# Kernel tuning notes

Hardware: AMD Instinct MI355X
Metric: run time of the kernel (lower is better)

## Reference

```python
import jax, jax.numpy as jnp
import numpy as np

C_IN = 256
K = 4
C_QK = C_IN // K  # 64


def setup_inputs() -> dict:
    key = jax.random.key(0)
    ks = jax.random.split(key, 9)
    B, C, H, W = 4, C_IN, 64, 64
    s = 0.02
    return {
        "x": jax.random.normal(ks[0], (B, C, H, W), dtype=jnp.float32),
        # 1x1 convs stored as dense [out, in] matrices (kernel_size=1)
        "wq": jax.random.normal(ks[1], (C_QK, C), dtype=jnp.float32) * s,
        "bq": jax.random.normal(ks[2], (C_QK,), dtype=jnp.float32) * s,
        "wk": jax.random.normal(ks[3], (C_QK, C), dtype=jnp.float32) * s,
        "bk": jax.random.normal(ks[4], (C_QK,), dtype=jnp.float32) * s,
        "wv": jax.random.normal(ks[5], (C, C), dtype=jnp.float32) * s,
        "bv": jax.random.normal(ks[6], (C,), dtype=jnp.float32) * s,
        "wg": jax.random.normal(ks[7], (C, C), dtype=jnp.float32) * s,
        "bg": jax.random.normal(ks[8], (C,), dtype=jnp.float32) * s,
    }


def reference(x, wq, bq, wk, bk, wv, bv, wg, bg):
    B, C, H, W = x.shape
    N = H * W
    xf = x.reshape(B, C, N)  # [B, C, N]
    # 1x1 conv == per-pixel linear over channels
    q = jnp.einsum("oc,bcn->bon", wq, xf) + bq[None, :, None]  # [B, Cqk, N]
    k = jnp.einsum("oc,bcn->bon", wk, xf) + bk[None, :, None]  # [B, Cqk, N]
    v = jnp.einsum("oc,bcn->bon", wv, xf) + bv[None, :, None]  # [B, C, N]
    # energy[b, n, m] = <q[:, n], k[:, m]>  (n = query pos, m = key pos)
    energy = jnp.einsum("bon,bom->bnm", q, k)  # [B, N, N]
    energy = jax.nn.elu(energy) / N
    # out[b, c, m] = sum_n v[b, c, n] * energy[b, n, m]
    out = jnp.einsum("bcn,bnm->bcm", v, energy).reshape(B, C, H, W)
    out = jnp.einsum("oc,bchw->bohw", wg, out) + bg[None, :, None, None]
    return out
```

## Files before the change

### kernel.cpp

```cpp
#include <hip/hip_runtime.h>

#define B_ 4
#define C_ 256
#define CQK 64
#define N_ 4096
#define SEG 2
#define SEGN (N_ / SEG)
#define NB 128
#define ITERS (SEGN / NB)
#define TS 512

typedef _Float16 f16;
typedef __attribute__((ext_vector_type(8))) _Float16 f16x8;
typedef __attribute__((ext_vector_type(4))) _Float16 f16x4;
typedef __attribute__((ext_vector_type(4))) float f32x4;
typedef __attribute__((ext_vector_type(4))) float float4v;

#define TILE_OFF(l15, quad) ((l15) * 32 + (quad) * 8)

__global__ __launch_bounds__(256) void prep_w(
    const float* __restrict__ wq, const float* __restrict__ wk,
    const float* __restrict__ wv, const float* __restrict__ wg,
    f16* __restrict__ WQt, f16* __restrict__ WKt, f16* __restrict__ WVt,
    f16* __restrict__ WGt) {
  int chunk = blockIdx.x * 256 + threadIdx.x;
  if (chunk >= 20480) return;
  const float* src;
  f16* dst;
  int lo;
  if (chunk < 2048) { src = wq; dst = WQt; lo = chunk * 8; }
  else if (chunk < 4096) { src = wk; dst = WKt; lo = (chunk - 2048) * 8; }
  else if (chunk < 12288) { src = wv; dst = WVt; lo = (chunk - 4096) * 8; }
  else { src = wg; dst = WGt; lo = (chunk - 12288) * 8; }
  int o = lo >> 8, k = lo & 255;
  f16x8 v;
#pragma unroll
  for (int j = 0; j < 8; j++) v[j] = (f16)src[lo + j];
  *(f16x8*)(dst + ((size_t)(o >> 4) * 8 + (k >> 5)) * TS + (o & 15) * 32 + (k & 31)) = v;
}

__global__ __launch_bounds__(256) void proj(
    const float* __restrict__ x, const f16* __restrict__ WQt,
    const f16* __restrict__ WKt, const f16* __restrict__ WVt,
    const float* __restrict__ bq, const float* __restrict__ bk,
    const float* __restrict__ bv, f16* __restrict__ QTt, f16* __restrict__ KTt,
    f16* __restrict__ Vt) {
  __shared__ float xs[32][257];
  __shared__ f16 xt[2][8][16 * 36];
  int nx = blockIdx.x;
  int n0 = nx * 32;
  int b = blockIdx.y;
  int tid = threadIdx.x, lane = tid & 63, w = tid >> 6;
  int l15 = lane & 15, quad = lane >> 4;
  const float* xb = x + (size_t)b * C_ * N_;

  {
    int a = tid & 7;
    int crow = tid >> 3;
#pragma unroll
    for (int p = 0; p < 8; p++) {
      int c = p * 32 + crow;
      float4v vv = *(const float4v*)(xb + (size_t)c * N_ + n0 + a * 4);
      int nn = a * 4;
      xs[nn][c] = vv[0];
      xs[nn + 1][c] = vv[1];
      xs[nn + 2][c] = vv[2];
      xs[nn + 3][c] = vv[3];
    }
  }
  __syncthreads();
#pragma unroll
  for (int nt = 0; nt < 2; nt++) {
#pragma unroll
    for (int kk = 0; kk < 2; kk++) {
      int kt = 2 * w + kk;
      f16x8 v;
#pragma unroll
      for (int j = 0; j < 8; j++)
        v[j] = (f16)xs[16 * nt + l15][kt * 32 + quad * 8 + j];
      *(f16x8*)(&xt[nt][kt][l15 * 36 + quad * 8]) = v;
    }
  }
  __syncthreads();

  f32x4 acc[6][2];
#pragma unroll
  for (int j = 0; j < 6; j++)
#pragma unroll
    for (int nt = 0; nt < 2; nt++) acc[j][nt] = (f32x4){0.f, 0.f, 0.f, 0.f};

#pragma unroll
  for (int kt = 0; kt < 8; kt++) {
    f16x8 xf[2];
#pragma unroll
    for (int nt = 0; nt < 2; nt++)
      xf[nt] = *(const f16x8*)(&xt[nt][kt][l15 * 36 + quad * 8]);
#pragma unroll
    for (int j = 0; j < 6; j++) {
      int g = w * 6 + j;
      const f16* Wt;
      int ot;
      bool isV = g < 16;
      if (isV) { Wt = WVt; ot = g; }
      else if (g < 20) { Wt = WQt; ot = g - 16; }
      else { Wt = WKt; ot = g - 20; }
      f16x8 wf = *(const f16x8*)(Wt + ((size_t)ot * 8 + kt) * TS + TILE_OFF(l15, quad));
#pragma unroll
      for (int nt = 0; nt < 2; nt++)
        acc[j][nt] = isV
            ? __builtin_amdgcn_mfma_f32_16x16x32_f16(xf[nt], wf, acc[j][nt], 0, 0, 0)
            : __builtin_amdgcn_mfma_f32_16x16x32_f16(wf, xf[nt], acc[j][nt], 0, 0, 0);
    }
  }

  f16* vbout = Vt + (size_t)b * C_ * N_;
#pragma unroll
  for (int j = 0; j < 6; j++) {
    int g = w * 6 + j;
    if (g < 16) {
      float bvv = bv[16 * g + l15];
#pragma unroll
      for (int nt = 0; nt < 2; nt++) {
        f16x4 vals;
#pragma unroll
        for (int r = 0; r < 4; r++) vals[r] = (f16)(acc[j][nt][r] + bvv);
        *(f16x4*)(vbout + ((size_t)g * 128 + nx) * TS + l15 * 32 + 16 * nt +
                  4 * quad) = vals;
      }
    } else {
      int oq = (g < 20) ? (g - 16) : (g - 20);
      const float* bias = (g < 20) ? bq : bk;
      f16* ob = ((g < 20) ? QTt : KTt) + (size_t)b * N_ * CQK;
#pragma unroll
      for (int nt = 0; nt < 2; nt++) {
        f16x4 vals;
#pragma unroll
        for (int r = 0; r < 4; r++)
          vals[r] = (f16)(acc[j][nt][r] + bias[16 * oq + 4 * quad + r]);
        *(f16x4*)(ob + ((size_t)(2 * nx + nt) * 2 + (oq >> 1)) * TS + l15 * 32 +
                  16 * (oq & 1) + 4 * quad) = vals;
      }
    }
  }
}

__global__ __launch_bounds__(256, 2) void attn(const f16* __restrict__ qt,
                                               const f16* __restrict__ kt,
                                               const f16* __restrict__ v,
                                               const f16* __restrict__ WGt,
                                               f16* __restrict__ part) {
  __shared__ __align__(16) f16 sPt[2][64][128];
  int m0 = blockIdx.x * 64;
  int seg = blockIdx.y;
  int b = blockIdx.z;
  int tid = threadIdx.x, lane = tid & 63, w = tid >> 6;
  int l15 = lane & 15, quad = lane >> 4;
  const f16* qtb = qt + (size_t)b * N_ * CQK;
  const f16* ktb = kt + (size_t)b * N_ * CQK;
  const f16* vb = v + (size_t)b * C_ * N_;

  f32x4 oacc[4][4];
#pragma unroll
  for (int ct = 0; ct < 4; ct++)
#pragma unroll
    for (int mt = 0; mt < 4; mt++) oacc[ct][mt] = (f32x4){0.f, 0.f, 0.f, 0.f};

  f16x8 kf[4][2];
#pragma unroll
  for (int mt = 0; mt < 4; mt++)
#pragma unroll
    for (int ks = 0; ks < 2; ks++)
      kf[mt][ks] = *(const f16x8*)(ktb + ((size_t)((m0 >> 4) + mt) * 2 + ks) * TS +
                                   TILE_OFF(l15, quad));

  f16x8 qf[2][2];
  {
    int nq = seg * SEGN;
#pragma unroll
    for (int nt = 0; nt < 2; nt++)
#pragma unroll
      for (int ks = 0; ks < 2; ks++)
        qf[nt][ks] = *(const f16x8*)(qtb +
                                     ((size_t)((nq >> 4) + 2 * w + nt) * 2 + ks) * TS +
                                     TILE_OFF(l15, quad));
  }

  for (int it = 0; it < ITERS; it++) {
    int n0 = seg * SEGN + it * NB;
    f16x8 vfA[2][4];
#pragma unroll
    for (int ks = 0; ks < 2; ks++)
#pragma unroll
      for (int ct = 0; ct < 4; ct++)
        vfA[ks][ct] = *(const f16x8*)(vb +
                                      ((size_t)(4 * w + ct) * 128 + (n0 >> 5) + ks) * TS +
                                      TILE_OFF(l15, quad));

    char* buf = (char*)sPt[it & 1];
#pragma unroll
    for (int nt = 0; nt < 2; nt++) {
      f32x4 sacc[4];
#pragma unroll
      for (int mt = 0; mt < 4; mt++) sacc[mt] = (f32x4){0.f, 0.f, 0.f, 0.f};
#pragma unroll
      for (int ks = 0; ks < 2; ks++)
#pragma unroll
        for (int mt = 0; mt < 4; mt++)
          sacc[mt] = __builtin_amdgcn_mfma_f32_16x16x32_f16(qf[nt][ks], kf[mt][ks],
                                                            sacc[mt], 0, 0, 0);
#pragma unroll
      for (int mt = 0; mt < 4; mt++) {
        f16x4 p;
#pragma unroll
        for (int r = 0; r < 4; r++) {
          float s = sacc[mt][r];
          p[r] = (f16)(s > 0.0f ? s : (__expf(s) - 1.0f));
        }
        int row = 16 * mt + l15;
        int colb = (64 * w + 32 * nt + 8 * quad) ^ ((row & 7) << 4);
        *(f16x4*)(buf + row * 256 + colb) = p;
      }
    }
    __syncthreads();

    f16x8 vfB[2][4];
    f16x8 pa[4];
#pragma unroll
    for (int mt = 0; mt < 4; mt++) {
      int row = 16 * mt + l15;
      pa[mt] = *(const f16x8*)(buf + row * 256 + ((quad * 16) ^ ((row & 7) << 4)));
    }
#pragma unroll
    for (int ks = 0; ks < 2; ks++)
#pragma unroll
      for (int ct = 0; ct < 4; ct++)
        vfB[ks][ct] = *(const f16x8*)(vb + ((size_t)(4 * w + ct) * 128 + (n0 >> 5) +
                                            2 + ks) * TS +
                                      TILE_OFF(l15, quad));
#pragma unroll
    for (int ct = 0; ct < 4; ct++)
#pragma unroll
      for (int mt = 0; mt < 4; mt++)
        oacc[ct][mt] = __builtin_amdgcn_mfma_f32_16x16x32_f16(vfA[0][ct], pa[mt],
                                                              oacc[ct][mt], 0, 0, 0);
    if (it + 1 < ITERS) {
      int nq = n0 + NB;
#pragma unroll
      for (int nt = 0; nt < 2; nt++)
#pragma unroll
        for (int ks = 0; ks < 2; ks++)
          qf[nt][ks] = *(const f16x8*)(qtb +
                                       ((size_t)((nq >> 4) + 2 * w + nt) * 2 + ks) * TS +
                                       TILE_OFF(l15, quad));
    }
#pragma unroll
    for (int mt = 0; mt < 4; mt++) {
      int row = 16 * mt + l15;
      pa[mt] = *(const f16x8*)(buf + row * 256 + ((64 + quad * 16) ^ ((row & 7) << 4)));
    }
#pragma unroll
    for (int ct = 0; ct < 4; ct++)
#pragma unroll
      for (int mt = 0; mt < 4; mt++)
        oacc[ct][mt] = __builtin_amdgcn_mfma_f32_16x16x32_f16(vfA[1][ct], pa[mt],
                                                              oacc[ct][mt], 0, 0, 0);
#pragma unroll
    for (int mt = 0; mt < 4; mt++) {
      int row = 16 * mt + l15;
      pa[mt] = *(const f16x8*)(buf + row * 256 + ((128 + quad * 16) ^ ((row & 7) << 4)));
    }
#pragma unroll
    for (int ct = 0; ct < 4; ct++)
#pragma unroll
      for (int mt = 0; mt < 4; mt++)
        oacc[ct][mt] = __builtin_amdgcn_mfma_f32_16x16x32_f16(vfB[0][ct], pa[mt],
                                                              oacc[ct][mt], 0, 0, 0);
#pragma unroll
    for (int mt = 0; mt < 4; mt++) {
      int row = 16 * mt + l15;
      pa[mt] = *(const f16x8*)(buf + row * 256 + ((192 + quad * 16) ^ ((row & 7) << 4)));
    }
#pragma unroll
    for (int ct = 0; ct < 4; ct++)
#pragma unroll
      for (int mt = 0; mt < 4; mt++)
        oacc[ct][mt] = __builtin_amdgcn_mfma_f32_16x16x32_f16(vfB[1][ct], pa[mt],
                                                              oacc[ct][mt], 0, 0, 0);
  }

  __syncthreads();
  f16* obuf = (f16*)sPt;
#pragma unroll
  for (int ct = 0; ct < 4; ct++) {
#pragma unroll
    for (int mt = 0; mt < 4; mt++) {
      f16x4 vals;
#pragma unroll
      for (int r = 0; r < 4; r++)
        vals[r] = (f16)(oacc[ct][mt][r] * (1.0f / (float)N_));
      *(f16x4*)(obuf + (mt * 8 + 2 * w + (ct >> 1)) * TS + l15 * 32 +
                16 * (ct & 1) + 4 * quad) = vals;
    }
  }
  __syncthreads();
  f32x4 accO[4][4];
#pragma unroll
  for (int ot = 0; ot < 4; ot++)
#pragma unroll
    for (int mt = 0; mt < 4; mt++) accO[ot][mt] = (f32x4){0.f, 0.f, 0.f, 0.f};
#pragma unroll
  for (int kt = 0; kt < 8; kt++) {
    f16x8 bO[4];
#pragma unroll
    for (int mt = 0; mt < 4; mt++)
      bO[mt] = *(const f16x8*)(obuf + (mt * 8 + kt) * TS + TILE_OFF(l15, quad));
#pragma unroll
    for (int ot = 0; ot < 4; ot++) {
      f16x8 af = *(const f16x8*)(WGt + ((size_t)(4 * w + ot) * 8 + kt) * TS +
                                 TILE_OFF(l15, quad));
#pragma unroll
      for (int mt = 0; mt < 4; mt++)
        accO[ot][mt] = __builtin_amdgcn_mfma_f32_16x16x32_f16(af, bO[mt], accO[ot][mt], 0, 0, 0);
    }
  }
  f16* pb = part + ((size_t)(seg * B_ + b) * C_) * N_;
#pragma unroll
  for (int ot = 0; ot < 4; ot++) {
#pragma unroll
    for (int mt = 0; mt < 4; mt++) {
      int m = m0 + 16 * mt + l15;
#pragma unroll
      for (int r = 0; r < 4; r++) {
        int o = 64 * w + 16 * ot + 4 * quad + r;
        pb[(size_t)o * N_ + m] = (f16)accO[ot][mt][r];
      }
    }
  }
}

__global__ __launch_bounds__(256) void combine(const f16* __restrict__ part,
                                               const float* __restrict__ bg,
                                               float* __restrict__ out) {
  size_t i = ((size_t)blockIdx.x * 256 + threadIdx.x) * 8;
  f16x8 p0 = *(const f16x8*)(part + i);
  f16x8 p1 = *(const f16x8*)(part + (size_t)B_ * C_ * N_ + i);
  float bgo = bg[(i >> 12) & 255];
  float4v r0, r1;
#pragma unroll
  for (int j = 0; j < 4; j++) r0[j] = (float)p0[j] + (float)p1[j] + bgo;
#pragma unroll
  for (int j = 0; j < 4; j++) r1[j] = (float)p0[4 + j] + (float)p1[4 + j] + bgo;
  *(float4v*)(out + i) = r0;
  *(float4v*)(out + i + 4) = r1;
}

extern "C" void kernel_launch(void* const* d_in, const int* in_sizes, int n_in,
                              void* d_out, int out_size, void* d_ws, size_t ws_size,
                              hipStream_t stream) {
  const float* x = (const float*)d_in[0];
  const float* wq = (const float*)d_in[1];
  const float* bq = (const float*)d_in[2];
  const float* wk = (const float*)d_in[3];
  const float* bk = (const float*)d_in[4];
  const float* wv = (const float*)d_in[5];
  const float* bv = (const float*)d_in[6];
  const float* wg = (const float*)d_in[7];
  const float* bg = (const float*)d_in[8];
  float* out = (float*)d_out;

  char* ws = (char*)d_ws;
  f16* QTt = (f16*)ws; ws += (size_t)B_ * N_ * CQK * sizeof(f16);
  f16* KTt = (f16*)ws; ws += (size_t)B_ * N_ * CQK * sizeof(f16);
  f16* Vt  = (f16*)ws; ws += (size_t)B_ * C_ * N_ * sizeof(f16);
  f16* WQt = (f16*)ws; ws += (size_t)CQK * C_ * sizeof(f16);
  f16* WKt = (f16*)ws; ws += (size_t)CQK * C_ * sizeof(f16);
  f16* WVt = (f16*)ws; ws += (size_t)C_ * C_ * sizeof(f16);
  f16* WGt = (f16*)ws; ws += (size_t)C_ * C_ * sizeof(f16);
  f16* PART = (f16*)ws; ws += (size_t)SEG * B_ * C_ * N_ * sizeof(f16);

  prep_w<<<dim3(80), 256, 0, stream>>>(wq, wk, wv, wg, WQt, WKt, WVt, WGt);
  proj<<<dim3(N_ / 32, B_), 256, 0, stream>>>(x, WQt, WKt, WVt, bq, bk, bv,
                                              QTt, KTt, Vt);
  attn<<<dim3(N_ / 64, SEG, B_), 256, 0, stream>>>(QTt, KTt, Vt, WGt, PART);
  combine<<<dim3(2048), 256, 0, stream>>>(PART, bg, out);
}
```

Measured before the change: 164.5 us.

## Drop weight prep kernel and process two key chunks per barrier in attention

Removes the separate prep_w launch. proj and attn now read the fp32 weights directly and convert them to f16 fragments inline. The attention main loop is unrolled by two: scores for two 128-wide n-chunks are computed into a 4-deep shared buffer before a single __syncthreads, which halves barrier count and gives more room to overlap V loads with MFMA work. In exchange it raises register pressure from the extra Q and V fragments, doubles LDS use, and adds redundant fp32 weight loads and conversions in every block.

```diff
diff --git a/kernel.cpp b/kernel.cpp
--- a/kernel.cpp
+++ b/kernel.cpp
@@ -18,30 +18,18 @@
 
 #define TILE_OFF(l15, quad) ((l15) * 32 + (quad) * 8)
 
-__global__ __launch_bounds__(256) void prep_w(
-    const float* __restrict__ wq, const float* __restrict__ wk,
-    const float* __restrict__ wv, const float* __restrict__ wg,
-    f16* __restrict__ WQt, f16* __restrict__ WKt, f16* __restrict__ WVt,
-    f16* __restrict__ WGt) {
-  int chunk = blockIdx.x * 256 + threadIdx.x;
-  if (chunk >= 20480) return;
-  const float* src;
-  f16* dst;
-  int lo;
-  if (chunk < 2048) { src = wq; dst = WQt; lo = chunk * 8; }
-  else if (chunk < 4096) { src = wk; dst = WKt; lo = (chunk - 2048) * 8; }
-  else if (chunk < 12288) { src = wv; dst = WVt; lo = (chunk - 4096) * 8; }
-  else { src = wg; dst = WGt; lo = (chunk - 12288) * 8; }
-  int o = lo >> 8, k = lo & 255;
-  f16x8 v;
-#pragma unroll
-  for (int j = 0; j < 8; j++) v[j] = (f16)src[lo + j];
-  *(f16x8*)(dst + ((size_t)(o >> 4) * 8 + (k >> 5)) * TS + (o & 15) * 32 + (k & 31)) = v;
+__device__ __forceinline__ f16x8 ldw_f32(const float* __restrict__ Wp) {
+  float4v a0 = *(const float4v*)Wp;
+  float4v a1 = *(const float4v*)(Wp + 4);
+  f16x8 r;
+#pragma unroll
+  for (int j = 0; j < 4; j++) { r[j] = (f16)a0[j]; r[4 + j] = (f16)a1[j]; }
+  return r;
 }
 
 __global__ __launch_bounds__(256) void proj(
-    const float* __restrict__ x, const f16* __restrict__ WQt,
-    const f16* __restrict__ WKt, const f16* __restrict__ WVt,
+    const float* __restrict__ x, const float* __restrict__ wq,
+    const float* __restrict__ wk, const float* __restrict__ wv,
     const float* __restrict__ bq, const float* __restrict__ bk,
     const float* __restrict__ bv, f16* __restrict__ QTt, f16* __restrict__ KTt,
     f16* __restrict__ Vt) {
@@ -98,13 +86,13 @@
 #pragma unroll
     for (int j = 0; j < 6; j++) {
       int g = w * 6 + j;
-      const f16* Wt;
-      int ot;
+      const float* Wsrc;
+      int orow;
       bool isV = g < 16;
-      if (isV) { Wt = WVt; ot = g; }
-      else if (g < 20) { Wt = WQt; ot = g - 16; }
-      else { Wt = WKt; ot = g - 20; }
-      f16x8 wf = *(const f16x8*)(Wt + ((size_t)ot * 8 + kt) * TS + TILE_OFF(l15, quad));
+      if (isV) { Wsrc = wv; orow = 16 * g + l15; }
+      else if (g < 20) { Wsrc = wq; orow = 16 * (g - 16) + l15; }
+      else { Wsrc = wk; orow = 16 * (g - 20) + l15; }
+      f16x8 wf = ldw_f32(Wsrc + (size_t)orow * C_ + kt * 32 + quad * 8);
 #pragma unroll
       for (int nt = 0; nt < 2; nt++)
         acc[j][nt] = isV
@@ -147,9 +135,9 @@
 __global__ __launch_bounds__(256, 2) void attn(const f16* __restrict__ qt,
                                                const f16* __restrict__ kt,
                                                const f16* __restrict__ v,
-                                               const f16* __restrict__ WGt,
+                                               const float* __restrict__ wg,
                                                f16* __restrict__ part) {
-  __shared__ __align__(16) f16 sPt[2][64][128];
+  __shared__ __align__(16) f16 sPt[4][64][128];
   int m0 = blockIdx.x * 64;
   int seg = blockIdx.y;
   int b = blockIdx.z;
@@ -173,30 +161,35 @@
       kf[mt][ks] = *(const f16x8*)(ktb + ((size_t)((m0 >> 4) + mt) * 2 + ks) * TS +
                                    TILE_OFF(l15, quad));
 
-  f16x8 qf[2][2];
+  f16x8 qf[2][2][2];
   {
-    int nq = seg * SEGN;
-#pragma unroll
-    for (int nt = 0; nt < 2; nt++)
-#pragma unroll
-      for (int ks = 0; ks < 2; ks++)
-        qf[nt][ks] = *(const f16x8*)(qtb +
-                                     ((size_t)((nq >> 4) + 2 * w + nt) * 2 + ks) * TS +
-                                     TILE_OFF(l15, quad));
-  }
-
-  for (int it = 0; it < ITERS; it++) {
+    int base = (seg * SEGN) >> 4;
+#pragma unroll
+    for (int cc = 0; cc < 2; cc++)
+#pragma unroll
+      for (int nt = 0; nt < 2; nt++)
+#pragma unroll
+        for (int ks = 0; ks < 2; ks++)
+          qf[cc][nt][ks] =
+              *(const f16x8*)(qtb + ((size_t)(base + cc * 8 + 2 * w + nt) * 2 + ks) * TS +
+                              TILE_OFF(l15, quad));
+  }
+
+  for (int it2 = 0; it2 < ITERS / 2; it2++) {
+    int it = 2 * it2;
     int n0 = seg * SEGN + it * NB;
-    f16x8 vfA[2][4];
+    int nc = n0 >> 5;
+    char* buf0 = (char*)sPt[it & 3];
+    char* buf1 = (char*)sPt[(it + 1) & 3];
+
+    f16x8 vA0[2][4];
 #pragma unroll
     for (int ks = 0; ks < 2; ks++)
 #pragma unroll
       for (int ct = 0; ct < 4; ct++)
-        vfA[ks][ct] = *(const f16x8*)(vb +
-                                      ((size_t)(4 * w + ct) * 128 + (n0 >> 5) + ks) * TS +
+        vA0[ks][ct] = *(const f16x8*)(vb + ((size_t)(4 * w + ct) * 128 + nc + ks) * TS +
                                       TILE_OFF(l15, quad));
 
-    char* buf = (char*)sPt[it & 1];
 #pragma unroll
     for (int nt = 0; nt < 2; nt++) {
       f32x4 sacc[4];
@@ -206,7 +199,7 @@
       for (int ks = 0; ks < 2; ks++)
 #pragma unroll
         for (int mt = 0; mt < 4; mt++)
-          sacc[mt] = __builtin_amdgcn_mfma_f32_16x16x32_f16(qf[nt][ks], kf[mt][ks],
+          sacc[mt] = __builtin_amdgcn_mfma_f32_16x16x32_f16(qf[0][nt][ks], kf[mt][ks],
                                                             sacc[mt], 0, 0, 0);
 #pragma unroll
       for (int mt = 0; mt < 4; mt++) {
@@ -218,73 +211,159 @@
         }
         int row = 16 * mt + l15;
         int colb = (64 * w + 32 * nt + 8 * quad) ^ ((row & 7) << 4);
-        *(f16x4*)(buf + row * 256 + colb) = p;
+        *(f16x4*)(buf0 + row * 256 + colb) = p;
       }
     }
+
+    f16x8 vB0[2][4];
+#pragma unroll
+    for (int ks = 0; ks < 2; ks++)
+#pragma unroll
+      for (int ct = 0; ct < 4; ct++)
+        vB0[ks][ct] = *(const f16x8*)(vb + ((size_t)(4 * w + ct) * 128 + nc + 2 + ks) * TS +
+                                      TILE_OFF(l15, quad));
+
+#pragma unroll
+    for (int nt = 0; nt < 2; nt++) {
+      f32x4 sacc[4];
+#pragma unroll
+      for (int mt = 0; mt < 4; mt++) sacc[mt] = (f32x4){0.f, 0.f, 0.f, 0.f};
+#pragma unroll
+      for (int ks = 0; ks < 2; ks++)
+#pragma unroll
+        for (int mt = 0; mt < 4; mt++)
+          sacc[mt] = __builtin_amdgcn_mfma_f32_16x16x32_f16(qf[1][nt][ks], kf[mt][ks],
+                                                            sacc[mt], 0, 0, 0);
+#pragma unroll
+      for (int mt = 0; mt < 4; mt++) {
+        f16x4 p;
+#pragma unroll
+        for (int r = 0; r < 4; r++) {
+          float s = sacc[mt][r];
+          p[r] = (f16)(s > 0.0f ? s : (__expf(s) - 1.0f));
+        }
+        int row = 16 * mt + l15;
+        int colb = (64 * w + 32 * nt + 8 * quad) ^ ((row & 7) << 4);
+        *(f16x4*)(buf1 + row * 256 + colb) = p;
+      }
+    }
     __syncthreads();
 
-    f16x8 vfB[2][4];
     f16x8 pa[4];
-#pragma unroll
-    for (int mt = 0; mt < 4; mt++) {
-      int row = 16 * mt + l15;
-      pa[mt] = *(const f16x8*)(buf + row * 256 + ((quad * 16) ^ ((row & 7) << 4)));
+    f16x8 vA1[2][4];
+#pragma unroll
+    for (int mt = 0; mt < 4; mt++) {
+      int row = 16 * mt + l15;
+      pa[mt] = *(const f16x8*)(buf0 + row * 256 + ((quad * 16) ^ ((row & 7) << 4)));
     }
 #pragma unroll
     for (int ks = 0; ks < 2; ks++)
 #pragma unroll
       for (int ct = 0; ct < 4; ct++)
-        vfB[ks][ct] = *(const f16x8*)(vb + ((size_t)(4 * w + ct) * 128 + (n0 >> 5) +
-                                            2 + ks) * TS +
+        vA1[ks][ct] = *(const f16x8*)(vb + ((size_t)(4 * w + ct) * 128 + nc + 4 + ks) * TS +
                                       TILE_OFF(l15, quad));
 #pragma unroll
     for (int ct = 0; ct < 4; ct++)
 #pragma unroll
       for (int mt = 0; mt < 4; mt++)
-        oacc[ct][mt] = __builtin_amdgcn_mfma_f32_16x16x32_f16(vfA[0][ct], pa[mt],
-                                                              oacc[ct][mt], 0, 0, 0);
-    if (it + 1 < ITERS) {
-      int nq = n0 + NB;
-#pragma unroll
-      for (int nt = 0; nt < 2; nt++)
-#pragma unroll
-        for (int ks = 0; ks < 2; ks++)
-          qf[nt][ks] = *(const f16x8*)(qtb +
-                                       ((size_t)((nq >> 4) + 2 * w + nt) * 2 + ks) * TS +
-                                       TILE_OFF(l15, quad));
-    }
-#pragma unroll
-    for (int mt = 0; mt < 4; mt++) {
-      int row = 16 * mt + l15;
-      pa[mt] = *(const f16x8*)(buf + row * 256 + ((64 + quad * 16) ^ ((row & 7) << 4)));
-    }
-#pragma unroll
-    for (int ct = 0; ct < 4; ct++)
-#pragma unroll
-      for (int mt = 0; mt < 4; mt++)
-        oacc[ct][mt] = __builtin_amdgcn_mfma_f32_16x16x32_f16(vfA[1][ct], pa[mt],
-                                                              oacc[ct][mt], 0, 0, 0);
-#pragma unroll
-    for (int mt = 0; mt < 4; mt++) {
-      int row = 16 * mt + l15;
-      pa[mt] = *(const f16x8*)(buf + row * 256 + ((128 + quad * 16) ^ ((row & 7) << 4)));
-    }
-#pragma unroll
-    for (int ct = 0; ct < 4; ct++)
-#pragma unroll
-      for (int mt = 0; mt < 4; mt++)
-        oacc[ct][mt] = __builtin_amdgcn_mfma_f32_16x16x32_f16(vfB[0][ct], pa[mt],
-                                                              oacc[ct][mt], 0, 0, 0);
-#pragma unroll
-    for (int mt = 0; mt < 4; mt++) {
-      int row = 16 * mt + l15;
-      pa[mt] = *(const f16x8*)(buf + row * 256 + ((192 + quad * 16) ^ ((row & 7) << 4)));
-    }
-#pragma unroll
-    for (int ct = 0; ct < 4; ct++)
-#pragma unroll
-      for (int mt = 0; mt < 4; mt++)
-        oacc[ct][mt] = __builtin_amdgcn_mfma_f32_16x16x32_f16(vfB[1][ct], pa[mt],
+        oacc[ct][mt] = __builtin_amdgcn_mfma_f32_16x16x32_f16(vA0[0][ct], pa[mt],
+                                                              oacc[ct][mt], 0, 0, 0);
+    if (it2 + 1 < ITERS / 2) {
+      int base = ((seg * SEGN) >> 4) + (it + 2) * 8;
+#pragma unroll
+      for (int cc = 0; cc < 2; cc++)
+#pragma unroll
+        for (int nt = 0; nt < 2; nt++)
+#pragma unroll
+          for (int ks = 0; ks < 2; ks++)
+            qf[cc][nt][ks] =
+                *(const f16x8*)(qtb + ((size_t)(base + cc * 8 + 2 * w + nt) * 2 + ks) * TS +
+                                TILE_OFF(l15, quad));
+    }
+#pragma unroll
+    for (int mt = 0; mt < 4; mt++) {
+      int row = 16 * mt + l15;
+      pa[mt] = *(const f16x8*)(buf0 + row * 256 + ((64 + quad * 16) ^ ((row & 7) << 4)));
+    }
+#pragma unroll
+    for (int ct = 0; ct < 4; ct++)
+#pragma unroll
+      for (int mt = 0; mt < 4; mt++)
+        oacc[ct][mt] = __builtin_amdgcn_mfma_f32_16x16x32_f16(vA0[1][ct], pa[mt],
+                                                              oacc[ct][mt], 0, 0, 0);
+#pragma unroll
+    for (int mt = 0; mt < 4; mt++) {
+      int row = 16 * mt + l15;
+      pa[mt] = *(const f16x8*)(buf0 + row * 256 + ((128 + quad * 16) ^ ((row & 7) << 4)));
+    }
+#pragma unroll
+    for (int ct = 0; ct < 4; ct++)
+#pragma unroll
+      for (int mt = 0; mt < 4; mt++)
+        oacc[ct][mt] = __builtin_amdgcn_mfma_f32_16x16x32_f16(vB0[0][ct], pa[mt],
+                                                              oacc[ct][mt], 0, 0, 0);
+    f16x8 vB1[2][4];
+#pragma unroll
+    for (int ks = 0; ks < 2; ks++)
+#pragma unroll
+      for (int ct = 0; ct < 4; ct++)
+        vB1[ks][ct] = *(const f16x8*)(vb + ((size_t)(4 * w + ct) * 128 + nc + 6 + ks) * TS +
+                                      TILE_OFF(l15, quad));
+#pragma unroll
+    for (int mt = 0; mt < 4; mt++) {
+      int row = 16 * mt + l15;
+      pa[mt] = *(const f16x8*)(buf0 + row * 256 + ((192 + quad * 16) ^ ((row & 7) << 4)));
+    }
+#pragma unroll
+    for (int ct = 0; ct < 4; ct++)
+#pragma unroll
+      for (int mt = 0; mt < 4; mt++)
+        oacc[ct][mt] = __builtin_amdgcn_mfma_f32_16x16x32_f16(vB0[1][ct], pa[mt],
+                                                              oacc[ct][mt], 0, 0, 0);
+
+#pragma unroll
+    for (int mt = 0; mt < 4; mt++) {
+      int row = 16 * mt + l15;
+      pa[mt] = *(const f16x8*)(buf1 + row * 256 + ((quad * 16) ^ ((row & 7) << 4)));
+    }
+#pragma unroll
+    for (int ct = 0; ct < 4; ct++)
+#pragma unroll
+      for (int mt = 0; mt < 4; mt++)
+        oacc[ct][mt] = __builtin_amdgcn_mfma_f32_16x16x32_f16(vA1[0][ct], pa[mt],
+                                                              oacc[ct][mt], 0, 0, 0);
+#pragma unroll
+    for (int mt = 0; mt < 4; mt++) {
+      int row = 16 * mt + l15;
+      pa[mt] = *(const f16x8*)(buf1 + row * 256 + ((64 + quad * 16) ^ ((row & 7) << 4)));
+    }
+#pragma unroll
+    for (int ct = 0; ct < 4; ct++)
+#pragma unroll
+      for (int mt = 0; mt < 4; mt++)
+        oacc[ct][mt] = __builtin_amdgcn_mfma_f32_16x16x32_f16(vA1[1][ct], pa[mt],
+                                                              oacc[ct][mt], 0, 0, 0);
+#pragma unroll
+    for (int mt = 0; mt < 4; mt++) {
+      int row = 16 * mt + l15;
+      pa[mt] = *(const f16x8*)(buf1 + row * 256 + ((128 + quad * 16) ^ ((row & 7) << 4)));
+    }
+#pragma unroll
+    for (int ct = 0; ct < 4; ct++)
+#pragma unroll
+      for (int mt = 0; mt < 4; mt++)
+        oacc[ct][mt] = __builtin_amdgcn_mfma_f32_16x16x32_f16(vB1[0][ct], pa[mt],
+                                                              oacc[ct][mt], 0, 0, 0);
+#pragma unroll
+    for (int mt = 0; mt < 4; mt++) {
+      int row = 16 * mt + l15;
+      pa[mt] = *(const f16x8*)(buf1 + row * 256 + ((192 + quad * 16) ^ ((row & 7) << 4)));
+    }
+#pragma unroll
+    for (int ct = 0; ct < 4; ct++)
+#pragma unroll
+      for (int mt = 0; mt < 4; mt++)
+        oacc[ct][mt] = __builtin_amdgcn_mfma_f32_16x16x32_f16(vB1[1][ct], pa[mt],
                                                               oacc[ct][mt], 0, 0, 0);
   }
 
@@ -316,8 +395,7 @@
       bO[mt] = *(const f16x8*)(obuf + (mt * 8 + kt) * TS + TILE_OFF(l15, quad));
 #pragma unroll
     for (int ot = 0; ot < 4; ot++) {
-      f16x8 af = *(const f16x8*)(WGt + ((size_t)(4 * w + ot) * 8 + kt) * TS +
-                                 TILE_OFF(l15, quad));
+      f16x8 af = ldw_f32(wg + (size_t)(64 * w + 16 * ot + l15) * C_ + kt * 32 + quad * 8);
 #pragma unroll
       for (int mt = 0; mt < 4; mt++)
         accO[ot][mt] = __builtin_amdgcn_mfma_f32_16x16x32_f16(af, bO[mt], accO[ot][mt], 0, 0, 0);
@@ -372,15 +450,10 @@
   f16* QTt = (f16*)ws; ws += (size_t)B_ * N_ * CQK * sizeof(f16);
   f16* KTt = (f16*)ws; ws += (size_t)B_ * N_ * CQK * sizeof(f16);
   f16* Vt  = (f16*)ws; ws += (size_t)B_ * C_ * N_ * sizeof(f16);
-  f16* WQt = (f16*)ws; ws += (size_t)CQK * C_ * sizeof(f16);
-  f16* WKt = (f16*)ws; ws += (size_t)CQK * C_ * sizeof(f16);
-  f16* WVt = (f16*)ws; ws += (size_t)C_ * C_ * sizeof(f16);
-  f16* WGt = (f16*)ws; ws += (size_t)C_ * C_ * sizeof(f16);
   f16* PART = (f16*)ws; ws += (size_t)SEG * B_ * C_ * N_ * sizeof(f16);
 
-  prep_w<<<dim3(80), 256, 0, stream>>>(wq, wk, wv, wg, WQt, WKt, WVt, WGt);
-  proj<<<dim3(N_ / 32, B_), 256, 0, stream>>>(x, WQt, WKt, WVt, bq, bk, bv,
+  proj<<<dim3(N_ / 32, B_), 256, 0, stream>>>(x, wq, wk, wv, bq, bk, bv,
                                               QTt, KTt, Vt);
-  attn<<<dim3(N_ / 64, SEG, B_), 256, 0, stream>>>(QTt, KTt, Vt, WGt, PART);
+  attn<<<dim3(N_ / 64, SEG, B_), 256, 0, stream>>>(QTt, KTt, Vt, wg, PART);
   combine<<<dim3(2048), 256, 0, stream>>>(PART, bg, out);
 }
```

Measured after the change: 188.6 us. +14.6%, slower.
